# Performance work log

Measured on AMD Instinct MI355X. Metric: run time of the kernel, lower is better.

Reference implementation:

```python
import jax, jax.numpy as jnp
import numpy as np

N = 50000        # num_nodes = user + item
D = 128          # latdim
L = 3            # gnn layers
R = 16           # hyper_rank
E = 1600000      # nnz of ts_drp_adj


def setup_inputs() -> dict:
    key = jax.random.key(0)
    ks = jax.random.split(key, 13)
    s = 1.0 / np.sqrt(D)
    return {
        "adj_rows": jax.random.randint(ks[0], (E,), 0, N, dtype=jnp.int32),
        "adj_cols": jax.random.randint(ks[1], (E,), 0, N, dtype=jnp.int32),
        "adj_vals": jax.random.uniform(ks[2], (E,), jnp.float32) * 0.05,
        "node_feats": jax.random.normal(ks[3], (N, D), jnp.float32) * s,
        "gnn_W": jax.random.normal(ks[4], (L, D, D), jnp.float32) * s,
        "gnn_b": jax.random.normal(ks[5], (L, D), jnp.float32) * 0.01,
        "fc1_W": jax.random.normal(ks[6], (D, D), jnp.float32) * s,
        "fc1_b": jax.random.normal(ks[7], (D,), jnp.float32) * 0.01,
        "fcrow_W": jax.random.normal(ks[8], (N * R, D), jnp.float32) * s,
        "fcrow_b": jax.random.normal(ks[9], (N * R,), jnp.float32) * 0.01,
        "fccol_W": jax.random.normal(ks[10], (R * D, D), jnp.float32) * s,
        "fccol_b": jax.random.normal(ks[11], (R * D,), jnp.float32) * 0.01,
        "ini_embeds": jax.random.normal(ks[12], (N, D), jnp.float32) * s,
    }


def _spmm(rows, cols, vals, h):
    # out[i] = sum_{e: rows[e]==i} vals[e] * h[cols[e]]   -- sparse adj @ h
    return jax.ops.segment_sum(vals[:, None] * h[cols], rows, num_segments=N)


def reference(adj_rows, adj_cols, adj_vals, node_feats, gnn_W, gnn_b,
              fc1_W, fc1_b, fcrow_W, fcrow_b, fccol_W, fccol_b, ini_embeds):
    h = node_feats
    h_sum = h  # running sum of layer outputs (residual mean-pool)
    for l in range(L):
        agg = _spmm(adj_rows, adj_cols, adj_vals, h)           # (N, D)
        h = jax.nn.elu(agg @ gnn_W[l].T + gnn_b[l])            # linear + ELU
        h_sum = h_sum + h
    h_bar = h_sum / (L + 1)
    z = h_bar.mean(axis=0)                                     # (D,)
    # Hypernetwork: z -> low-rank W_u = W_row @ W_col
    hz = jax.nn.leaky_relu(z @ fc1_W.T + fc1_b, negative_slope=0.2)
    W_row = (hz @ fcrow_W.T + fcrow_b).reshape(N, R)
    W_col = (hz @ fccol_W.T + fccol_b).reshape(R, D)
    W_u = W_row @ W_col                                        # (N, D)
    tuned_emb = ini_embeds + W_u * ini_embeds
    return tuned_emb
```

## Files before the change

### kernel.cpp

```cpp
#include <hip/hip_runtime.h>
#include <hip/hip_bf16.h>
#include <math.h>

#define NN 50000
#define DD 128
#define LLAYERS 3
#define RR 16
#define EE 1600000

typedef unsigned int u32;

__device__ __forceinline__ float bflo(u32 u){ union{u32 i;float f;}a; a.i=u<<16; return a.f; }
__device__ __forceinline__ float bfhi(u32 u){ union{u32 i;float f;}a; a.i=u&0xffff0000u; return a.f; }
__device__ __forceinline__ u32 pack_bf2(float x, float y){
  union{float f;u32 i;}a,b; a.f=x; b.f=y;
  u32 xr = (a.i + 0x7fffu + ((a.i>>16)&1u)) >> 16;
  u32 yr = (b.i + 0x7fffu + ((b.i>>16)&1u)) & 0xffff0000u;
  return (xr & 0xffffu) | yr;
}

__global__ __launch_bounds__(256) void k_hist(const int* __restrict__ rows, int* __restrict__ cnt){
  int e = blockIdx.x*256 + threadIdx.x;
  if (e < EE) atomicAdd(&cnt[rows[e]], 1);
}

__global__ __launch_bounds__(256) void k_scanA(const int* __restrict__ cnt, int* __restrict__ bsum){
  __shared__ int s[256];
  int i = blockIdx.x*256 + threadIdx.x;
  int v = (i < NN) ? ((cnt[i]+7)&~7) : 0;
  s[threadIdx.x] = v; __syncthreads();
  for (int off=128; off>0; off>>=1){
    if (threadIdx.x < off) s[threadIdx.x] += s[threadIdx.x+off];
    __syncthreads();
  }
  if (threadIdx.x==0) bsum[blockIdx.x] = s[0];
}

__global__ __launch_bounds__(256) void k_scanB(int* bsum){
  __shared__ int s[256];
  int t = threadIdx.x;
  int v = bsum[t];
  s[t] = v; __syncthreads();
  for (int off=1; off<256; off<<=1){
    int x = (t>=off) ? s[t-off] : 0; __syncthreads();
    s[t] += x; __syncthreads();
  }
  bsum[t] = s[t] - v;
}

__global__ __launch_bounds__(256) void k_scanC(const int* __restrict__ cnt, const int* __restrict__ bsum,
                        int* __restrict__ row_ptr, int* __restrict__ cursor,
                        int2* __restrict__ colval){
  __shared__ int s[256];
  int t = threadIdx.x; int i = blockIdx.x*256 + t;
  int n = (i<NN)?cnt[i]:0;
  int v = (n+7)&~7;
  s[t]=v; __syncthreads();
  for (int off=1; off<256; off<<=1){
    int x=(t>=off)?s[t-off]:0; __syncthreads();
    s[t]+=x; __syncthreads();
  }
  if (i<NN){
    int e = bsum[blockIdx.x] + s[t]-v;
    row_ptr[i]=e; cursor[i]=e;
    int2 z0; z0.x=0; z0.y=0;
    for (int p=e+n; p<e+v; ++p) colval[p] = z0;
    if (i == NN-1){
      for (int p=e+v; p<e+v+128; ++p) colval[p] = z0;
    }
  }
}

__global__ __launch_bounds__(256) void k_scatter(const int* __restrict__ rows, const int* __restrict__ cols,
                          const float* __restrict__ vals,
                          int* __restrict__ cursor, int2* __restrict__ colval){
  int e = blockIdx.x*256+threadIdx.x;
  if (e<EE){
    int r = rows[e];
    int p = atomicAdd(&cursor[r],1);
    int2 cv; cv.x = cols[e]; cv.y = __float_as_int(vals[e]);
    colval[p] = cv;
  }
}

__global__ __launch_bounds__(256) void k_initwT(const float4* __restrict__ nf, uint2* __restrict__ hbf,
                                                float* __restrict__ z,
                                                const float* __restrict__ W, float* __restrict__ wT){
  __shared__ float zp[128];
  int t = threadIdx.x;
  if (t < 128) zp[t] = 0.f;
  if (blockIdx.x < 192){
    int idx = blockIdx.x*256+t;
    int l = idx >> 14; int r = idx & 16383; int k = r >> 7; int j = r & 127;
    wT[(l<<14) + k*128 + j] = W[(l<<14) + j*128 + k];
  }
  float a0=0.f,a1=0.f,a2=0.f,a3=0.f;
  for (int i = blockIdx.x*256 + t; i < NN*DD/4; i += gridDim.x*256){
    float4 v = nf[i];
    uint2 p; p.x = pack_bf2(v.x, v.y); p.y = pack_bf2(v.z, v.w);
    hbf[i] = p;
    a0 += v.x; a1 += v.y; a2 += v.z; a3 += v.w;
  }
  __syncthreads();
  int c = (t*4) & 127;
  atomicAdd(&zp[c],a0); atomicAdd(&zp[c+1],a1); atomicAdd(&zp[c+2],a2); atomicAdd(&zp[c+3],a3);
  __syncthreads();
  if (t < 128) atomicAdd(&z[((blockIdx.x&15)<<7) + t], zp[t]);
}

#define FMA8(v, h)                                         \
  a0 = fmaf(v, bflo(h.x), a0); a1 = fmaf(v, bfhi(h.x), a1);\
  a2 = fmaf(v, bflo(h.y), a2); a3 = fmaf(v, bfhi(h.y), a3);\
  a4 = fmaf(v, bflo(h.z), a4); a5 = fmaf(v, bfhi(h.z), a5);\
  a6 = fmaf(v, bflo(h.w), a6); a7 = fmaf(v, bfhi(h.w), a7);

__global__ __launch_bounds__(256) void k_layer(const int* __restrict__ row_ptr, const int* __restrict__ cnt,
                       const int2* __restrict__ colval,
                       const u32* __restrict__ hin, const float* __restrict__ wTl,
                       const float* __restrict__ bl,
                       u32* __restrict__ hout, float* __restrict__ z, int last){
  __shared__ float a_s[16*128];
  __shared__ float w_s[32*128];
  __shared__ float zp[128];
  int t = threadIdx.x;
  if (t < 128) zp[t] = 0.f;
  int i0 = blockIdx.x * 16;
  int lane = t & 63;
  int wv = t >> 6;
  int sub = lane >> 4, k = lane & 15;

  for (int r = 0; r < 4; ++r){
    int row = i0 + wv*4 + r;
    int base = row_ptr[row], n = cnt[row];
    int iters = (n + 7) >> 3;
    const int2* cvp = colval + base + sub;
    float a0=0,a1=0,a2=0,a3=0,a4=0,a5=0,a6=0,a7=0;

    int2 c0a = cvp[0],  c0b = cvp[4];
    int2 c1a = cvp[8],  c1b = cvp[12];
    uint4 h0a = *(const uint4*)&hin[((size_t)(u32)c0a.x<<6) + (k<<2)];
    uint4 h0b = *(const uint4*)&hin[((size_t)(u32)c0b.x<<6) + (k<<2)];

    for (int it = 0; it < iters; ++it){
      int2 c2a = cvp[16], c2b = cvp[20];
      uint4 h1a = *(const uint4*)&hin[((size_t)(u32)c1a.x<<6) + (k<<2)];
      uint4 h1b = *(const uint4*)&hin[((size_t)(u32)c1b.x<<6) + (k<<2)];
      float v0 = __int_as_float(c0a.y);
      float v1 = __int_as_float(c0b.y);
      FMA8(v0, h0a);
      FMA8(v1, h0b);
      c0a = c1a; c0b = c1b; c1a = c2a; c1b = c2b;
      h0a = h1a; h0b = h1b;
      cvp += 8;
    }

    a0 += __shfl_xor(a0,16); a0 += __shfl_xor(a0,32);
    a1 += __shfl_xor(a1,16); a1 += __shfl_xor(a1,32);
    a2 += __shfl_xor(a2,16); a2 += __shfl_xor(a2,32);
    a3 += __shfl_xor(a3,16); a3 += __shfl_xor(a3,32);
    a4 += __shfl_xor(a4,16); a4 += __shfl_xor(a4,32);
    a5 += __shfl_xor(a5,16); a5 += __shfl_xor(a5,32);
    a6 += __shfl_xor(a6,16); a6 += __shfl_xor(a6,32);
    a7 += __shfl_xor(a7,16); a7 += __shfl_xor(a7,32);
    if (sub==0){
      float4 o0; o0.x=a0; o0.y=a1; o0.z=a2; o0.w=a3;
      float4 o1; o1.x=a4; o1.y=a5; o1.z=a6; o1.w=a7;
      *(float4*)&a_s[(wv*4+r)*128 + k*8] = o0;
      *(float4*)&a_s[(wv*4+r)*128 + k*8 + 4] = o1;
    }
  }
  __syncthreads();

  int jj = lane*2;
  float b0 = bl[jj], b1 = bl[jj+1];
  float acc[4][2];
  #pragma unroll
  for (int r=0;r<4;r++){ acc[r][0]=b0; acc[r][1]=b1; }
  for (int ch=0; ch<4; ++ch){
    const float4* wsrc = (const float4*)(wTl + ch*32*128);
    float4* wdst = (float4*)w_s;
    wdst[t]     = wsrc[t];
    wdst[t+256] = wsrc[t+256];
    wdst[t+512] = wsrc[t+512];
    wdst[t+768] = wsrc[t+768];
    __syncthreads();
    #pragma unroll 4
    for (int kk=0;kk<32;kk++){
      float2 w2 = *(const float2*)&w_s[kk*128 + jj];
      int kg = ch*32 + kk;
      #pragma unroll
      for (int r=0;r<4;r++){
        float a = a_s[(wv*4+r)*128 + kg];
        acc[r][0] = fmaf(a, w2.x, acc[r][0]);
        acc[r][1] = fmaf(a, w2.y, acc[r][1]);
      }
    }
    __syncthreads();
  }
  float zc0 = 0.f, zc1 = 0.f;
  #pragma unroll
  for (int r=0;r<4;r++){
    int row = i0 + wv*4 + r;
    float e0 = acc[r][0] > 0.f ? acc[r][0] : expm1f(acc[r][0]);
    float e1 = acc[r][1] > 0.f ? acc[r][1] : expm1f(acc[r][1]);
    zc0 += e0; zc1 += e1;
    if (!last)
      hout[(size_t)row*64 + (jj>>1)] = pack_bf2(e0, e1);
  }
  atomicAdd(&zp[jj], zc0); atomicAdd(&zp[jj+1], zc1);
  __syncthreads();
  if (t < 128) atomicAdd(&z[((blockIdx.x&15)<<7) + t], zp[t]);
}

__global__ __launch_bounds__(256) void k_hzwcol(const float* __restrict__ z, const float* __restrict__ fc1W,
                     const float* __restrict__ fc1b, float* __restrict__ hzg,
                     const float* __restrict__ Wc, const float* __restrict__ bc,
                     float* __restrict__ wcol){
  __shared__ float zs[128];
  __shared__ float hzs[128];
  int t = threadIdx.x;
  if (t < 128){
    float s = 0.f;
    #pragma unroll
    for (int q=0;q<16;q++) s += z[(q<<7) + t];
    zs[t] = s * (1.0f / (4.0f * (float)NN));
  }
  __syncthreads();
  if (t < 128){
    float acc = fc1b[t];
    const float* wr = &fc1W[t*128];
    #pragma unroll 8
    for (int k=0;k<128;k++)
      acc = fmaf(zs[k], wr[k], acc);
    float h = acc >= 0.f ? acc : 0.2f*acc;
    hzs[t] = h;
    if (blockIdx.x==0) hzg[t] = h;
  }
  __syncthreads();
  int m = blockIdx.x*256 + t;
  float acc = bc[m];
  const float* wr = &Wc[(size_t)m*128];
  #pragma unroll 8
  for (int k=0;k<128;k++)
    acc = fmaf(hzs[k], wr[k], acc);
  wcol[m] = acc;
}

__global__ __launch_bounds__(256) void k_wrowfinal(const float* __restrict__ hz, const float* __restrict__ W,
                        const float* __restrict__ b, const float* __restrict__ wcol,
                        const float* __restrict__ ini, float* __restrict__ out){
  __shared__ float wc[16*128];
  int t = threadIdx.x;
  ((float4*)wc)[t] = ((const float4*)wcol)[t];
  ((float4*)wc)[t+256] = ((const float4*)wcol)[t+256];
  __syncthreads();
  int lane = t & 63;
  int i = (blockIdx.x*256 + t) >> 6;
  int h = lane >> 5;
  int kq = lane & 31;
  float4 hzv = *(const float4*)&hz[kq*4];
  const float4* wp = (const float4*)(W + (size_t)i*16*128);
  const float* bp = b + (size_t)i*16;
  float wr8[8];
  #pragma unroll
  for (int q=0;q<8;q++){
    float4 wv = wp[q*64 + lane];
    float p = wv.x*hzv.x;
    p = fmaf(wv.y, hzv.y, p);
    p = fmaf(wv.z, hzv.z, p);
    p = fmaf(wv.w, hzv.w, p);
    p += __shfl_xor(p,1); p += __shfl_xor(p,2); p += __shfl_xor(p,4);
    p += __shfl_xor(p,8); p += __shfl_xor(p,16);
    wr8[q] = p + bp[2*q + h];
  }
  int c = lane*2;
  float a0=0.f, a1=0.f;
  #pragma unroll
  for (int q=0;q<8;q++){
    float we = wr8[q];
    float wo = __shfl_xor(wr8[q], 32);
    const float2 cA = *(const float2*)&wc[(2*q+h)*128 + c];
    const float2 cB = *(const float2*)&wc[(2*q+1-h)*128 + c];
    a0 = fmaf(we, cA.x, a0); a1 = fmaf(we, cA.y, a1);
    a0 = fmaf(wo, cB.x, a0); a1 = fmaf(wo, cB.y, a1);
  }
  float2 e = *(const float2*)&ini[(size_t)i*128 + c];
  float2 o; o.x = e.x*(1.f+a0); o.y = e.y*(1.f+a1);
  *(float2*)&out[(size_t)i*128 + c] = o;
}

extern "C" void kernel_launch(void* const* d_in, const int* in_sizes, int n_in,
                              void* d_out, int out_size, void* d_ws, size_t ws_size,
                              hipStream_t stream) {
  const int* adj_rows = (const int*)d_in[0];
  const int* adj_cols = (const int*)d_in[1];
  const float* adj_vals = (const float*)d_in[2];
  const float* node_feats = (const float*)d_in[3];
  const float* gnn_W = (const float*)d_in[4];
  const float* gnn_b = (const float*)d_in[5];
  const float* fc1_W = (const float*)d_in[6];
  const float* fc1_b = (const float*)d_in[7];
  const float* fcrow_W = (const float*)d_in[8];
  const float* fcrow_b = (const float*)d_in[9];
  const float* fccol_W = (const float*)d_in[10];
  const float* fccol_b = (const float*)d_in[11];
  const float* ini = (const float*)d_in[12];
  float* out = (float*)d_out;

  char* w = (char*)d_ws;
  auto alloc = [&](size_t bytes)->void*{ void* p = (void*)w; w += (bytes + 255) & ~(size_t)255; return p; };
  int*   cnt    = (int*)  alloc((size_t)NN*4);
  float* zb     = (float*)alloc(16*128*4);
  u32*   hbf_a  = (u32*)  alloc((size_t)NN*DD*2);
  u32*   hbf_b  = (u32*)  alloc((size_t)NN*DD*2);
  int2*  colval = (int2*) alloc(((size_t)EE + 8*NN + 256)*8);
  int*   row_ptr= (int*)  alloc((size_t)NN*4);
  int*   cursor = (int*)  alloc((size_t)NN*4);
  int*   bsum   = (int*)  alloc(256*4);
  float* wT     = (float*)alloc(3*128*128*4);
  float* hzb    = (float*)alloc(128*4);
  float* wcolb  = (float*)alloc(2048*4);

  hipMemsetAsync(cnt, 0, ((NN*4 + 255) & ~(size_t)255) + 16*128*4, stream);

  k_hist<<<EE/256, 256, 0, stream>>>(adj_rows, cnt);
  k_scanA<<<256, 256, 0, stream>>>(cnt, bsum);
  k_scanB<<<1, 256, 0, stream>>>(bsum);
  k_scanC<<<256, 256, 0, stream>>>(cnt, bsum, row_ptr, cursor, colval);
  k_scatter<<<EE/256, 256, 0, stream>>>(adj_rows, adj_cols, adj_vals, cursor, colval);
  k_initwT<<<400, 256, 0, stream>>>((const float4*)node_feats, (uint2*)hbf_a, zb, gnn_W, wT);

  const u32* hin = hbf_a; u32* hout = hbf_b;
  for (int l=0; l<LLAYERS; ++l){
    k_layer<<<NN/16, 256, 0, stream>>>(row_ptr, cnt, colval, hin, wT + l*16384,
                                       gnn_b + l*128, hout, zb, (l==LLAYERS-1) ? 1 : 0);
    const u32* tmp = hin; hin = hout; hout = (u32*)tmp;
  }

  k_hzwcol<<<8, 256, 0, stream>>>(zb, fc1_W, fc1_b, hzb, fccol_W, fccol_b, wcolb);
  k_wrowfinal<<<NN/4, 256, 0, stream>>>(hzb, fcrow_W, fcrow_b, wcolb, ini, out);
}
```

Before: 1.033 ms.

## Rework SpMM gather to 32-lane halves with smaller weight tiles for occupancy

The per-row gather now splits each wavefront into two 32-lane halves, each handling alternating edges with 8-byte loads of 4 bf16 features, instead of four 16-lane groups using 16-byte loads. The software prefetch pipeline is removed. The weight staging tile in shared memory is halved to 16 rows per chunk, and launch bounds request 8 blocks per SM. Together these are meant to cut register and LDS use so more waves are resident to hide gather latency. The cost is narrower loads, fewer edges in flight per wave, and twice as many barrier-separated weight chunks.

```diff
diff --git a/kernel.cpp b/kernel.cpp
--- a/kernel.cpp
+++ b/kernel.cpp
@@ -108,65 +108,49 @@
   if (t < 128) atomicAdd(&z[((blockIdx.x&15)<<7) + t], zp[t]);
 }
 
-#define FMA8(v, h)                                         \
+#define FMA4(v, h)                                         \
   a0 = fmaf(v, bflo(h.x), a0); a1 = fmaf(v, bfhi(h.x), a1);\
-  a2 = fmaf(v, bflo(h.y), a2); a3 = fmaf(v, bfhi(h.y), a3);\
-  a4 = fmaf(v, bflo(h.z), a4); a5 = fmaf(v, bfhi(h.z), a5);\
-  a6 = fmaf(v, bflo(h.w), a6); a7 = fmaf(v, bfhi(h.w), a7);
-
-__global__ __launch_bounds__(256) void k_layer(const int* __restrict__ row_ptr, const int* __restrict__ cnt,
+  a2 = fmaf(v, bflo(h.y), a2); a3 = fmaf(v, bfhi(h.y), a3);
+
+__global__ __launch_bounds__(256, 8) void k_layer(const int* __restrict__ row_ptr, const int* __restrict__ cnt,
                        const int2* __restrict__ colval,
                        const u32* __restrict__ hin, const float* __restrict__ wTl,
                        const float* __restrict__ bl,
                        u32* __restrict__ hout, float* __restrict__ z, int last){
   __shared__ float a_s[16*128];
-  __shared__ float w_s[32*128];
+  __shared__ float w_s[16*128];
   __shared__ float zp[128];
   int t = threadIdx.x;
   if (t < 128) zp[t] = 0.f;
   int i0 = blockIdx.x * 16;
   int lane = t & 63;
   int wv = t >> 6;
-  int sub = lane >> 4, k = lane & 15;
+  int sub = lane >> 5, q = lane & 31;
 
   for (int r = 0; r < 4; ++r){
     int row = i0 + wv*4 + r;
     int base = row_ptr[row], n = cnt[row];
-    int iters = (n + 7) >> 3;
+    int iters = ((n + 7) & ~7) >> 2;
     const int2* cvp = colval + base + sub;
-    float a0=0,a1=0,a2=0,a3=0,a4=0,a5=0,a6=0,a7=0;
-
-    int2 c0a = cvp[0],  c0b = cvp[4];
-    int2 c1a = cvp[8],  c1b = cvp[12];
-    uint4 h0a = *(const uint4*)&hin[((size_t)(u32)c0a.x<<6) + (k<<2)];
-    uint4 h0b = *(const uint4*)&hin[((size_t)(u32)c0b.x<<6) + (k<<2)];
-
+    float a0=0,a1=0,a2=0,a3=0;
     for (int it = 0; it < iters; ++it){
-      int2 c2a = cvp[16], c2b = cvp[20];
-      uint4 h1a = *(const uint4*)&hin[((size_t)(u32)c1a.x<<6) + (k<<2)];
-      uint4 h1b = *(const uint4*)&hin[((size_t)(u32)c1b.x<<6) + (k<<2)];
-      float v0 = __int_as_float(c0a.y);
-      float v1 = __int_as_float(c0b.y);
-      FMA8(v0, h0a);
-      FMA8(v1, h0b);
-      c0a = c1a; c0b = c1b; c1a = c2a; c1b = c2b;
-      h0a = h1a; h0b = h1b;
-      cvp += 8;
+      int2 cv0 = cvp[0];
+      int2 cv1 = cvp[2];
+      uint2 h0 = *(const uint2*)&hin[((size_t)(u32)cv0.x<<6) + (q<<1)];
+      uint2 h1 = *(const uint2*)&hin[((size_t)(u32)cv1.x<<6) + (q<<1)];
+      float v0 = __int_as_float(cv0.y);
+      float v1 = __int_as_float(cv1.y);
+      FMA4(v0, h0);
+      FMA4(v1, h1);
+      cvp += 4;
     }
-
-    a0 += __shfl_xor(a0,16); a0 += __shfl_xor(a0,32);
-    a1 += __shfl_xor(a1,16); a1 += __shfl_xor(a1,32);
-    a2 += __shfl_xor(a2,16); a2 += __shfl_xor(a2,32);
-    a3 += __shfl_xor(a3,16); a3 += __shfl_xor(a3,32);
-    a4 += __shfl_xor(a4,16); a4 += __shfl_xor(a4,32);
-    a5 += __shfl_xor(a5,16); a5 += __shfl_xor(a5,32);
-    a6 += __shfl_xor(a6,16); a6 += __shfl_xor(a6,32);
-    a7 += __shfl_xor(a7,16); a7 += __shfl_xor(a7,32);
+    a0 += __shfl_xor(a0,32);
+    a1 += __shfl_xor(a1,32);
+    a2 += __shfl_xor(a2,32);
+    a3 += __shfl_xor(a3,32);
     if (sub==0){
-      float4 o0; o0.x=a0; o0.y=a1; o0.z=a2; o0.w=a3;
-      float4 o1; o1.x=a4; o1.y=a5; o1.z=a6; o1.w=a7;
-      *(float4*)&a_s[(wv*4+r)*128 + k*8] = o0;
-      *(float4*)&a_s[(wv*4+r)*128 + k*8 + 4] = o1;
+      float4 o; o.x=a0; o.y=a1; o.z=a2; o.w=a3;
+      *(float4*)&a_s[(wv*4+r)*128 + q*4] = o;
     }
   }
   __syncthreads();
@@ -176,18 +160,16 @@
   float acc[4][2];
   #pragma unroll
   for (int r=0;r<4;r++){ acc[r][0]=b0; acc[r][1]=b1; }
-  for (int ch=0; ch<4; ++ch){
-    const float4* wsrc = (const float4*)(wTl + ch*32*128);
+  for (int ch=0; ch<8; ++ch){
+    const float4* wsrc = (const float4*)(wTl + ch*16*128);
     float4* wdst = (float4*)w_s;
     wdst[t]     = wsrc[t];
     wdst[t+256] = wsrc[t+256];
-    wdst[t+512] = wsrc[t+512];
-    wdst[t+768] = wsrc[t+768];
     __syncthreads();
     #pragma unroll 4
-    for (int kk=0;kk<32;kk++){
+    for (int kk=0;kk<16;kk++){
       float2 w2 = *(const float2*)&w_s[kk*128 + jj];
-      int kg = ch*32 + kk;
+      int kg = ch*16 + kk;
       #pragma unroll
       for (int r=0;r<4;r++){
         float a = a_s[(wv*4+r)*128 + kg];
```

Result: slower. 1.098 ms (+6.2%).
